# Kernel optimization log

Hardware: AMD Instinct MI355X
Metric: run time of the kernel (lower is better)

## Reference

```python
import jax, jax.numpy as jnp
import numpy as np

D_MODEL = 256
N_HEADS = 8
D_K = D_MODEL // N_HEADS
N = 4096
N_SEG = 16


def setup_inputs() -> dict:
    key = jax.random.key(0)
    ks = jax.random.split(key, 12)
    s = 0.02
    x_q = jax.random.normal(ks[0], (N, D_MODEL), jnp.float32)
    x_kv = jax.random.normal(ks[1], (N, D_MODEL), jnp.float32)
    # same key -> identical segment ids so every query segment exists in kv
    batch = jnp.sort(jax.random.randint(ks[2], (N,), 0, N_SEG)).astype(jnp.int64)
    params = {}
    names = ['Wq', 'Wk', 'Wv', 'Wo']
    for i, n in enumerate(names):
        params[n] = jax.random.normal(ks[3 + i], (D_MODEL, D_MODEL), jnp.float32) * s
        params['b' + n[1]] = jnp.zeros((D_MODEL,), jnp.float32)
    return dict(x_q=x_q, x_kv=x_kv, batch_q=batch, batch_kv=batch, **params)


def reference(x_q, x_kv, batch_q, batch_kv, Wq, bq, Wk, bk, Wv, bv, Wo, bo):
    # projections (torch Linear: x @ W.T + b)
    q = (x_q @ Wq.T + bq).reshape(N, N_HEADS, D_K)   # [Nq, H, dk]
    k = (x_kv @ Wk.T + bk).reshape(N, N_HEADS, D_K)  # [Nkv, H, dk]
    v = (x_kv @ Wv.T + bv).reshape(N, N_HEADS, D_K)
    scores = jnp.einsum('qhd,khd->hqk', q, k) / jnp.sqrt(jnp.float32(D_K))
    mask = batch_q[:, None] == batch_kv[None, :]      # block-diagonal [Nq, Nkv]
    scores = jnp.where(mask[None], scores, -jnp.inf)
    attn = jax.nn.softmax(scores, axis=-1)            # [H, Nq, Nkv]
    out = jnp.einsum('hqk,khd->qhd', attn, v).reshape(N, D_MODEL)
    out = out @ Wo.T + bo
    return out, attn[None]  # match torch's [1, H, Nq, Nkv] attn shape
```

## Files before the change

kernel.cpp:

```cpp
#include <hip/hip_runtime.h>

#define N_TOK 4096
#define DM 256
#define NH 8
#define DK 32

using u16 = unsigned short;
using u32 = unsigned int;
using i64 = long long;
typedef float f32x4 __attribute__((ext_vector_type(4)));

__device__ __forceinline__ float bf2f(u16 u){ return __uint_as_float(((u32)u) << 16); }
__device__ __forceinline__ u16 f2bf(float f){
    u32 x = __float_as_uint(f);
    x += 0x7fffu + ((x >> 16) & 1u);
    return (u16)(x >> 16);
}

__global__ __launch_bounds__(256)
void wt_kernel(const float* __restrict__ Wq, const float* __restrict__ Wk,
               const float* __restrict__ Wv, const float* __restrict__ Wo,
               float* __restrict__ Tq, float* __restrict__ Tk,
               float* __restrict__ Tv, float* __restrict__ To,
               const void* __restrict__ batch_q, const void* __restrict__ batch_kv,
               int2* __restrict__ bounds)
{
    const int b = blockIdx.x;
    const int t = threadIdx.x;
    if (b < 64){
        const float* W = (b < 16) ? Wq : (b < 32) ? Wk : (b < 48) ? Wv : Wo;
        float*      T  = (b < 16) ? Tq : (b < 32) ? Tk : (b < 48) ? Tv : To;
        int blk = b & 15;
        float4* T4 = (float4*)T;
#pragma unroll
        for (int f = 0; f < 4; ++f){
            int F = blk * 1024 + f * 256 + t;
            int d4 = F >> 8;
            int c  = F & 255;
            float4 v = *(const float4*)(W + (size_t)c * DM + 4 * d4);
            T4[F] = v;
        }
    } else {
        int q = (b - 64) * 256 + t;
        const int* kv32 = (const int*)batch_kv;
        const i64* kv64 = (const i64*)batch_kv;
        bool is64 = (kv32[N_TOK - 1] == 0);
        int s = is64 ? (int)((const i64*)batch_q)[q] : ((const int*)batch_q)[q];
        int lo = 0, hi = N_TOK;
        while (lo < hi){ int m = (lo + hi) >> 1; int v = is64 ? (int)kv64[m] : kv32[m]; if (v < s) lo = m + 1; else hi = m; }
        int lo2 = lo, hi2 = N_TOK;
        while (lo2 < hi2){ int m = (lo2 + hi2) >> 1; int v = is64 ? (int)kv64[m] : kv32[m]; if (v <= s) lo2 = m + 1; else hi2 = m; }
        bounds[q] = make_int2(lo, lo2);
    }
}

__global__ __launch_bounds__(256)
void pre_kernel(const float* __restrict__ xq, const float* __restrict__ xkv,
                const float* __restrict__ Tq, const float* __restrict__ bq,
                const float* __restrict__ Tk, const float* __restrict__ bk,
                const float* __restrict__ Tv, const float* __restrict__ bv,
                float* __restrict__ Q, u16* __restrict__ Kp, u16* __restrict__ Vp)
{
    const int b = blockIdx.x;
    const int c = threadIdx.x;
    const int ROWS = 8;

    if (b < 512){
        int row0 = b * ROWS;
        float acc[ROWS];
        float bvv = bq[c];
#pragma unroll
        for (int r = 0; r < ROWS; ++r) acc[r] = bvv;
        const float4* T4 = (const float4*)Tq;
        const float4* xb = (const float4*)(xq + (size_t)row0 * DM);
        for (int i = 0; i < DM / 4; ++i){
            float4 w = T4[i * 256 + c];
#pragma unroll
            for (int r = 0; r < ROWS; ++r){
                float4 xv = xb[r * (DM / 4) + i];
                acc[r] += xv.x * w.x + xv.y * w.y + xv.z * w.z + xv.w * w.w;
            }
        }
#pragma unroll
        for (int r = 0; r < ROWS; ++r)
            Q[(size_t)(row0 + r) * DM + c] = acc[r];
    } else {
        int row0 = (b - 512) * ROWS;
        int hh = c >> 5, dd = c & 31;
        float acck[ROWS], accv[ROWS];
        float bkv = bk[c], bvv = bv[c];
#pragma unroll
        for (int r = 0; r < ROWS; ++r){ acck[r] = bkv; accv[r] = bvv; }
        const float4* Tk4 = (const float4*)Tk;
        const float4* Tv4 = (const float4*)Tv;
        const float4* xb  = (const float4*)(xkv + (size_t)row0 * DM);
        for (int i = 0; i < DM / 4; ++i){
            float4 wk = Tk4[i * 256 + c];
            float4 wv = Tv4[i * 256 + c];
#pragma unroll
            for (int r = 0; r < ROWS; ++r){
                float4 xv = xb[r * (DM / 4) + i];
                acck[r] += xv.x * wk.x + xv.y * wk.y + xv.z * wk.z + xv.w * wk.w;
                accv[r] += xv.x * wv.x + xv.y * wv.y + xv.z * wv.z + xv.w * wv.w;
            }
        }
#pragma unroll
        for (int r = 0; r < ROWS; ++r){
            size_t idx = ((size_t)hh * N_TOK + (row0 + r)) * DK + dd;
            Kp[idx] = f2bf(acck[r]);
            Vp[idx] = f2bf(accv[r]);
        }
    }
}

__global__ __launch_bounds__(256)
void proj_kernel(const float* __restrict__ x, const float* __restrict__ T,
                 const float* __restrict__ bias, float* __restrict__ out)
{
    const int ROWS = 8;
    int row0 = blockIdx.x * ROWS;
    int c = threadIdx.x;
    float acc[ROWS];
    float bv = bias[c];
#pragma unroll
    for (int r = 0; r < ROWS; ++r) acc[r] = bv;
    const float4* T4 = (const float4*)T;
    const float4* xb = (const float4*)(x + (size_t)row0 * DM);
    for (int i = 0; i < DM / 4; ++i){
        float4 w = T4[i * 256 + c];
#pragma unroll
        for (int r = 0; r < ROWS; ++r){
            float4 xv = xb[r * (DM / 4) + i];
            acc[r] += xv.x * w.x + xv.y * w.y + xv.z * w.z + xv.w * w.w;
        }
    }
#pragma unroll
    for (int r = 0; r < ROWS; ++r)
        out[(size_t)(row0 + r) * DM + c] = acc[r];
}

__global__ __launch_bounds__(256)
void attn_kernel(const float* __restrict__ Q, const u16* __restrict__ K,
                 const u16* __restrict__ V, const int2* __restrict__ bounds,
                 float* __restrict__ attn, float* __restrict__ O)
{
    __shared__ float sc[N_TOK];
    __shared__ float qs[DK];
    __shared__ float red[8];
    __shared__ float Osh[DK];

    int q = blockIdx.x, h = blockIdx.y, tid = threadIdx.x;
    int2 bnd = bounds[q];
    const int lo = bnd.x, hi = bnd.y;
    const u16* Kh = K + (size_t)h * N_TOK * DK;
    const u16* Vh = V + (size_t)h * N_TOK * DK;

    if (tid < DK){ qs[tid] = Q[(size_t)q * DM + h * DK + tid]; Osh[tid] = 0.f; }
    __syncthreads();

    const float scale = 0.17677669529663687f;

    float lmax = -1e30f;
    for (int k = lo + tid; k < hi; k += 256){
        const uint4* kr = (const uint4*)(Kh + (size_t)k * DK);
        float dot = 0.f;
#pragma unroll
        for (int i = 0; i < 4; ++i){
            uint4 p = kr[i];
            dot += qs[i*8+0]*bf2f((u16)p.x) + qs[i*8+1]*bf2f((u16)(p.x>>16));
            dot += qs[i*8+2]*bf2f((u16)p.y) + qs[i*8+3]*bf2f((u16)(p.y>>16));
            dot += qs[i*8+4]*bf2f((u16)p.z) + qs[i*8+5]*bf2f((u16)(p.z>>16));
            dot += qs[i*8+6]*bf2f((u16)p.w) + qs[i*8+7]*bf2f((u16)(p.w>>16));
        }
        dot *= scale;
        sc[k - lo] = dot;
        lmax = fmaxf(lmax, dot);
    }
#pragma unroll
    for (int off = 32; off; off >>= 1) lmax = fmaxf(lmax, __shfl_xor(lmax, off, 64));
    if ((tid & 63) == 0) red[tid >> 6] = lmax;
    __syncthreads();
    float m = fmaxf(fmaxf(red[0], red[1]), fmaxf(red[2], red[3]));

    float lsum = 0.f;
    for (int k = lo + tid; k < hi; k += 256){
        float p = __expf(sc[k - lo] - m);
        sc[k - lo] = p;
        lsum += p;
    }
#pragma unroll
    for (int off = 32; off; off >>= 1) lsum += __shfl_xor(lsum, off, 64);
    if ((tid & 63) == 0) red[4 + (tid >> 6)] = lsum;
    __syncthreads();
    float sum = red[4] + red[5] + red[6] + red[7];
    float inv = (sum > 0.f) ? (1.0f / sum) : 0.f;

    f32x4* arow4 = (f32x4*)(attn + ((size_t)h * N_TOK + q) * N_TOK);
#pragma unroll
    for (int i = 0; i < N_TOK / 1024; ++i){
        int t = i * 256 + tid;
        int k0 = 4 * t;
        f32x4 w;
        w.x = (k0 + 0 >= lo && k0 + 0 < hi) ? sc[k0 + 0 - lo] * inv : 0.f;
        w.y = (k0 + 1 >= lo && k0 + 1 < hi) ? sc[k0 + 1 - lo] * inv : 0.f;
        w.z = (k0 + 2 >= lo && k0 + 2 < hi) ? sc[k0 + 2 - lo] * inv : 0.f;
        w.w = (k0 + 3 >= lo && k0 + 3 < hi) ? sc[k0 + 3 - lo] * inv : 0.f;
        __builtin_nontemporal_store(w, &arow4[t]);
    }

    int d2 = tid & 15;
    int g  = tid >> 4;
    float p0 = 0.f, p1 = 0.f;
    for (int k = lo + g; k < hi; k += 16){
        u32 pv = *(const u32*)(Vh + (size_t)k * DK + 2 * d2);
        float p = sc[k - lo];
        p0 += p * bf2f((u16)pv);
        p1 += p * bf2f((u16)(pv >> 16));
    }
    p0 += __shfl_xor(p0, 16, 64); p0 += __shfl_xor(p0, 32, 64);
    p1 += __shfl_xor(p1, 16, 64); p1 += __shfl_xor(p1, 32, 64);
    if ((tid & 63) < 16){
        atomicAdd(&Osh[2 * d2 + 0], p0);
        atomicAdd(&Osh[2 * d2 + 1], p1);
    }

    __syncthreads();
    if (tid < DK) O[(size_t)q * DM + h * DK + tid] = Osh[tid] * inv;
}

extern "C" void kernel_launch(void* const* d_in, const int* in_sizes, int n_in,
                              void* d_out, int out_size, void* d_ws, size_t ws_size,
                              hipStream_t stream)
{
    const float* x_q  = (const float*)d_in[0];
    const float* x_kv = (const float*)d_in[1];
    const void* batch_q  = d_in[2];
    const void* batch_kv = d_in[3];
    const float* Wq = (const float*)d_in[4];
    const float* bq = (const float*)d_in[5];
    const float* Wk = (const float*)d_in[6];
    const float* bk = (const float*)d_in[7];
    const float* Wv = (const float*)d_in[8];
    const float* bv = (const float*)d_in[9];
    const float* Wo = (const float*)d_in[10];
    const float* bo = (const float*)d_in[11];

    char* ws = (char*)d_ws;
    float* Q  = (float*)ws;
    u16*   Kp = (u16*)(ws + (size_t)4 * 1024 * 1024);
    u16*   Vp = (u16*)(ws + (size_t)6 * 1024 * 1024);
    float* O  = (float*)(ws + (size_t)8 * 1024 * 1024);
    int2* bounds = (int2*)(ws + (size_t)12 * 1024 * 1024);
    float* Tq = (float*)(ws + (size_t)13 * 1024 * 1024);
    float* Tk = (float*)(ws + (size_t)13 * 1024 * 1024 + 256 * 1024);
    float* Tv = (float*)(ws + (size_t)13 * 1024 * 1024 + 512 * 1024);
    float* To = (float*)(ws + (size_t)13 * 1024 * 1024 + 768 * 1024);

    float* out  = (float*)d_out;
    float* attn = out + (size_t)N_TOK * DM;

    wt_kernel<<<80, 256, 0, stream>>>(Wq, Wk, Wv, Wo, Tq, Tk, Tv, To,
                                      batch_q, batch_kv, bounds);
    pre_kernel<<<1024, 256, 0, stream>>>(x_q, x_kv, Tq, bq, Tk, bk, Tv, bv,
                                         Q, Kp, Vp);
    attn_kernel<<<dim3(N_TOK, NH), 256, 0, stream>>>(Q, Kp, Vp, bounds, attn, O);
    proj_kernel<<<N_TOK/8, 256, 0, stream>>>((const float*)O, To, bo, out);
}
```

Before: 673.9 us.

## Store K transposed in fp32 and split attn zero-fill from segment writes

The K projection is now written as an fp32 transposed [head*dim][token] array, so threads handling consecutive keys read contiguous floats with q held in registers, instead of unpacking bf16 rows. The attention-row store now writes zero vectors outside the segment range in separate loops and computes values only within the segment span. This trades double the K storage and bandwidth for coalesced access and simpler per-element logic.

```diff
diff --git a/kernel.cpp b/kernel.cpp
--- a/kernel.cpp
+++ b/kernel.cpp
@@ -59,7 +59,7 @@
                 const float* __restrict__ Tq, const float* __restrict__ bq,
                 const float* __restrict__ Tk, const float* __restrict__ bk,
                 const float* __restrict__ Tv, const float* __restrict__ bv,
-                float* __restrict__ Q, u16* __restrict__ Kp, u16* __restrict__ Vp)
+                float* __restrict__ Q, float* __restrict__ KT, u16* __restrict__ Vp)
 {
     const int b = blockIdx.x;
     const int c = threadIdx.x;
@@ -104,10 +104,12 @@
                 accv[r] += xv.x * wv.x + xv.y * wv.y + xv.z * wv.z + xv.w * wv.w;
             }
         }
+        float4* kt4 = (float4*)(KT + (size_t)c * N_TOK + row0);
+        kt4[0] = make_float4(acck[0], acck[1], acck[2], acck[3]);
+        kt4[1] = make_float4(acck[4], acck[5], acck[6], acck[7]);
 #pragma unroll
         for (int r = 0; r < ROWS; ++r){
             size_t idx = ((size_t)hh * N_TOK + (row0 + r)) * DK + dd;
-            Kp[idx] = f2bf(acck[r]);
             Vp[idx] = f2bf(accv[r]);
         }
     }
@@ -140,7 +142,7 @@
 }
 
 __global__ __launch_bounds__(256)
-void attn_kernel(const float* __restrict__ Q, const u16* __restrict__ K,
+void attn_kernel(const float* __restrict__ Q, const float* __restrict__ KT,
                  const u16* __restrict__ V, const int2* __restrict__ bounds,
                  float* __restrict__ attn, float* __restrict__ O)
 {
@@ -152,26 +154,24 @@
     int q = blockIdx.x, h = blockIdx.y, tid = threadIdx.x;
     int2 bnd = bounds[q];
     const int lo = bnd.x, hi = bnd.y;
-    const u16* Kh = K + (size_t)h * N_TOK * DK;
+    const float* KTh = KT + (size_t)h * DK * N_TOK;
     const u16* Vh = V + (size_t)h * N_TOK * DK;
 
     if (tid < DK){ qs[tid] = Q[(size_t)q * DM + h * DK + tid]; Osh[tid] = 0.f; }
     __syncthreads();
 
     const float scale = 0.17677669529663687f;
+
+    float qr[DK];
+#pragma unroll
+    for (int d = 0; d < DK; ++d) qr[d] = qs[d];
 
     float lmax = -1e30f;
     for (int k = lo + tid; k < hi; k += 256){
-        const uint4* kr = (const uint4*)(Kh + (size_t)k * DK);
         float dot = 0.f;
 #pragma unroll
-        for (int i = 0; i < 4; ++i){
-            uint4 p = kr[i];
-            dot += qs[i*8+0]*bf2f((u16)p.x) + qs[i*8+1]*bf2f((u16)(p.x>>16));
-            dot += qs[i*8+2]*bf2f((u16)p.y) + qs[i*8+3]*bf2f((u16)(p.y>>16));
-            dot += qs[i*8+4]*bf2f((u16)p.z) + qs[i*8+5]*bf2f((u16)(p.z>>16));
-            dot += qs[i*8+6]*bf2f((u16)p.w) + qs[i*8+7]*bf2f((u16)(p.w>>16));
-        }
+        for (int d = 0; d < DK; ++d)
+            dot += qr[d] * KTh[(size_t)d * N_TOK + k];
         dot *= scale;
         sc[k - lo] = dot;
         lmax = fmaxf(lmax, dot);
@@ -196,9 +196,14 @@
     float inv = (sum > 0.f) ? (1.0f / sum) : 0.f;
 
     f32x4* arow4 = (f32x4*)(attn + ((size_t)h * N_TOK + q) * N_TOK);
-#pragma unroll
-    for (int i = 0; i < N_TOK / 1024; ++i){
-        int t = i * 256 + tid;
+    const f32x4 z4 = {0.f, 0.f, 0.f, 0.f};
+    const int lo4 = lo >> 2;
+    const int hi4 = (hi + 3) >> 2;
+    for (int t = tid; t < lo4; t += 256)
+        __builtin_nontemporal_store(z4, &arow4[t]);
+    for (int t = hi4 + tid; t < N_TOK / 4; t += 256)
+        __builtin_nontemporal_store(z4, &arow4[t]);
+    for (int t = lo4 + tid; t < hi4; t += 256){
         int k0 = 4 * t;
         f32x4 w;
         w.x = (k0 + 0 >= lo && k0 + 0 < hi) ? sc[k0 + 0 - lo] * inv : 0.f;
@@ -247,14 +252,14 @@
 
     char* ws = (char*)d_ws;
     float* Q  = (float*)ws;
-    u16*   Kp = (u16*)(ws + (size_t)4 * 1024 * 1024);
-    u16*   Vp = (u16*)(ws + (size_t)6 * 1024 * 1024);
-    float* O  = (float*)(ws + (size_t)8 * 1024 * 1024);
-    int2* bounds = (int2*)(ws + (size_t)12 * 1024 * 1024);
-    float* Tq = (float*)(ws + (size_t)13 * 1024 * 1024);
-    float* Tk = (float*)(ws + (size_t)13 * 1024 * 1024 + 256 * 1024);
-    float* Tv = (float*)(ws + (size_t)13 * 1024 * 1024 + 512 * 1024);
-    float* To = (float*)(ws + (size_t)13 * 1024 * 1024 + 768 * 1024);
+    float* KT = (float*)(ws + (size_t)4 * 1024 * 1024);
+    u16*   Vp = (u16*)(ws + (size_t)8 * 1024 * 1024);
+    float* O  = (float*)(ws + (size_t)10 * 1024 * 1024);
+    int2* bounds = (int2*)(ws + (size_t)14 * 1024 * 1024);
+    float* Tq = (float*)(ws + (size_t)14 * 1024 * 1024 + 256 * 1024);
+    float* Tk = (float*)(ws + (size_t)14 * 1024 * 1024 + 512 * 1024);
+    float* Tv = (float*)(ws + (size_t)14 * 1024 * 1024 + 768 * 1024);
+    float* To = (float*)(ws + (size_t)14 * 1024 * 1024 + 1024 * 1024);
 
     float* out  = (float*)d_out;
     float* attn = out + (size_t)N_TOK * DM;
@@ -262,7 +267,7 @@
     wt_kernel<<<80, 256, 0, stream>>>(Wq, Wk, Wv, Wo, Tq, Tk, Tv, To,
                                       batch_q, batch_kv, bounds);
     pre_kernel<<<1024, 256, 0, stream>>>(x_q, x_kv, Tq, bq, Tk, bk, Tv, bv,
-                                         Q, Kp, Vp);
-    attn_kernel<<<dim3(N_TOK, NH), 256, 0, stream>>>(Q, Kp, Vp, bounds, attn, O);
+                                         Q, KT, Vp);
+    attn_kernel<<<dim3(N_TOK, NH), 256, 0, stream>>>(Q, KT, Vp, bounds, attn, O);
     proj_kernel<<<N_TOK/8, 256, 0, stream>>>((const float*)O, To, bo, out);
 }
```

New measurement: 697.5 us. 3.5% more time.

## Process all heads per query block and split zero-fill stores from softmax stores

Applied to the files above, without the earlier changes.

The attention kernel now launches one block per query instead of one per (query, head). Each block loops over the 8 heads, loading the full query row into shared memory once and holding the per-head slice in registers. The attention-row write is split into pure zero-fill loops outside the segment and a masked loop only over the segment's range, which avoids per-element LDS reads and bounds checks on the zeroed region. This cuts block count and launch granularity, but serialises the heads within a block, which may reduce latency hiding on the store-bound attention-matrix write.

```diff
diff --git a/kernel.cpp b/kernel.cpp
--- a/kernel.cpp
+++ b/kernel.cpp
@@ -145,87 +145,103 @@
                  float* __restrict__ attn, float* __restrict__ O)
 {
     __shared__ float sc[N_TOK];
-    __shared__ float qs[DK];
+    __shared__ float qs[DM];
     __shared__ float red[8];
     __shared__ float Osh[DK];
 
-    int q = blockIdx.x, h = blockIdx.y, tid = threadIdx.x;
-    int2 bnd = bounds[q];
+    const int q = blockIdx.x, tid = threadIdx.x;
+    const int2 bnd = bounds[q];
     const int lo = bnd.x, hi = bnd.y;
-    const u16* Kh = K + (size_t)h * N_TOK * DK;
-    const u16* Vh = V + (size_t)h * N_TOK * DK;
-
-    if (tid < DK){ qs[tid] = Q[(size_t)q * DM + h * DK + tid]; Osh[tid] = 0.f; }
+
+    if (tid < 64) ((float4*)qs)[tid] = ((const float4*)(Q + (size_t)q * DM))[tid];
+    if (tid < DK) Osh[tid] = 0.f;
     __syncthreads();
 
     const float scale = 0.17677669529663687f;
-
-    float lmax = -1e30f;
-    for (int k = lo + tid; k < hi; k += 256){
-        const uint4* kr = (const uint4*)(Kh + (size_t)k * DK);
-        float dot = 0.f;
-#pragma unroll
-        for (int i = 0; i < 4; ++i){
-            uint4 p = kr[i];
-            dot += qs[i*8+0]*bf2f((u16)p.x) + qs[i*8+1]*bf2f((u16)(p.x>>16));
-            dot += qs[i*8+2]*bf2f((u16)p.y) + qs[i*8+3]*bf2f((u16)(p.y>>16));
-            dot += qs[i*8+4]*bf2f((u16)p.z) + qs[i*8+5]*bf2f((u16)(p.z>>16));
-            dot += qs[i*8+6]*bf2f((u16)p.w) + qs[i*8+7]*bf2f((u16)(p.w>>16));
-        }
-        dot *= scale;
-        sc[k - lo] = dot;
-        lmax = fmaxf(lmax, dot);
-    }
-#pragma unroll
-    for (int off = 32; off; off >>= 1) lmax = fmaxf(lmax, __shfl_xor(lmax, off, 64));
-    if ((tid & 63) == 0) red[tid >> 6] = lmax;
-    __syncthreads();
-    float m = fmaxf(fmaxf(red[0], red[1]), fmaxf(red[2], red[3]));
-
-    float lsum = 0.f;
-    for (int k = lo + tid; k < hi; k += 256){
-        float p = __expf(sc[k - lo] - m);
-        sc[k - lo] = p;
-        lsum += p;
-    }
-#pragma unroll
-    for (int off = 32; off; off >>= 1) lsum += __shfl_xor(lsum, off, 64);
-    if ((tid & 63) == 0) red[4 + (tid >> 6)] = lsum;
-    __syncthreads();
-    float sum = red[4] + red[5] + red[6] + red[7];
-    float inv = (sum > 0.f) ? (1.0f / sum) : 0.f;
-
-    f32x4* arow4 = (f32x4*)(attn + ((size_t)h * N_TOK + q) * N_TOK);
-#pragma unroll
-    for (int i = 0; i < N_TOK / 1024; ++i){
-        int t = i * 256 + tid;
-        int k0 = 4 * t;
-        f32x4 w;
-        w.x = (k0 + 0 >= lo && k0 + 0 < hi) ? sc[k0 + 0 - lo] * inv : 0.f;
-        w.y = (k0 + 1 >= lo && k0 + 1 < hi) ? sc[k0 + 1 - lo] * inv : 0.f;
-        w.z = (k0 + 2 >= lo && k0 + 2 < hi) ? sc[k0 + 2 - lo] * inv : 0.f;
-        w.w = (k0 + 3 >= lo && k0 + 3 < hi) ? sc[k0 + 3 - lo] * inv : 0.f;
-        __builtin_nontemporal_store(w, &arow4[t]);
-    }
-
-    int d2 = tid & 15;
-    int g  = tid >> 4;
-    float p0 = 0.f, p1 = 0.f;
-    for (int k = lo + g; k < hi; k += 16){
-        u32 pv = *(const u32*)(Vh + (size_t)k * DK + 2 * d2);
-        float p = sc[k - lo];
-        p0 += p * bf2f((u16)pv);
-        p1 += p * bf2f((u16)(pv >> 16));
-    }
-    p0 += __shfl_xor(p0, 16, 64); p0 += __shfl_xor(p0, 32, 64);
-    p1 += __shfl_xor(p1, 16, 64); p1 += __shfl_xor(p1, 32, 64);
-    if ((tid & 63) < 16){
-        atomicAdd(&Osh[2 * d2 + 0], p0);
-        atomicAdd(&Osh[2 * d2 + 1], p1);
-    }
-
-    __syncthreads();
-    if (tid < DK) O[(size_t)q * DM + h * DK + tid] = Osh[tid] * inv;
+    const int lo4 = lo >> 2;
+    const int hi4 = (hi + 3) >> 2;
+
+    for (int h = 0; h < NH; ++h){
+        const u16* Kh = K + (size_t)h * N_TOK * DK;
+        const u16* Vh = V + (size_t)h * N_TOK * DK;
+
+        float qr[DK];
+#pragma unroll
+        for (int d = 0; d < DK; ++d) qr[d] = qs[h * DK + d];
+
+        float lmax = -1e30f;
+        for (int k = lo + tid; k < hi; k += 256){
+            const uint4* kr = (const uint4*)(Kh + (size_t)k * DK);
+            float dot = 0.f;
+#pragma unroll
+            for (int i = 0; i < 4; ++i){
+                uint4 p = kr[i];
+                dot += qr[i*8+0]*bf2f((u16)p.x) + qr[i*8+1]*bf2f((u16)(p.x>>16));
+                dot += qr[i*8+2]*bf2f((u16)p.y) + qr[i*8+3]*bf2f((u16)(p.y>>16));
+                dot += qr[i*8+4]*bf2f((u16)p.z) + qr[i*8+5]*bf2f((u16)(p.z>>16));
+                dot += qr[i*8+6]*bf2f((u16)p.w) + qr[i*8+7]*bf2f((u16)(p.w>>16));
+            }
+            dot *= scale;
+            sc[k - lo] = dot;
+            lmax = fmaxf(lmax, dot);
+        }
+#pragma unroll
+        for (int off = 32; off; off >>= 1) lmax = fmaxf(lmax, __shfl_xor(lmax, off, 64));
+        if ((tid & 63) == 0) red[tid >> 6] = lmax;
+        __syncthreads();
+        float m = fmaxf(fmaxf(red[0], red[1]), fmaxf(red[2], red[3]));
+
+        float lsum = 0.f;
+        for (int k = lo + tid; k < hi; k += 256){
+            float p = __expf(sc[k - lo] - m);
+            sc[k - lo] = p;
+            lsum += p;
+        }
+#pragma unroll
+        for (int off = 32; off; off >>= 1) lsum += __shfl_xor(lsum, off, 64);
+        if ((tid & 63) == 0) red[4 + (tid >> 6)] = lsum;
+        __syncthreads();
+        float sum = red[4] + red[5] + red[6] + red[7];
+        float inv = (sum > 0.f) ? (1.0f / sum) : 0.f;
+
+        f32x4* arow4 = (f32x4*)(attn + ((size_t)h * N_TOK + q) * N_TOK);
+        const f32x4 z4 = {0.f, 0.f, 0.f, 0.f};
+        for (int t = tid; t < lo4; t += 256)
+            __builtin_nontemporal_store(z4, &arow4[t]);
+        for (int t = hi4 + tid; t < N_TOK / 4; t += 256)
+            __builtin_nontemporal_store(z4, &arow4[t]);
+        for (int t = lo4 + tid; t < hi4; t += 256){
+            int k0 = 4 * t;
+            f32x4 w;
+            w.x = (k0 + 0 >= lo && k0 + 0 < hi) ? sc[k0 + 0 - lo] * inv : 0.f;
+            w.y = (k0 + 1 >= lo && k0 + 1 < hi) ? sc[k0 + 1 - lo] * inv : 0.f;
+            w.z = (k0 + 2 >= lo && k0 + 2 < hi) ? sc[k0 + 2 - lo] * inv : 0.f;
+            w.w = (k0 + 3 >= lo && k0 + 3 < hi) ? sc[k0 + 3 - lo] * inv : 0.f;
+            __builtin_nontemporal_store(w, &arow4[t]);
+        }
+
+        int d2 = tid & 15;
+        int g  = tid >> 4;
+        float p0 = 0.f, p1 = 0.f;
+        for (int k = lo + g; k < hi; k += 16){
+            u32 pv = *(const u32*)(Vh + (size_t)k * DK + 2 * d2);
+            float p = sc[k - lo];
+            p0 += p * bf2f((u16)pv);
+            p1 += p * bf2f((u16)(pv >> 16));
+        }
+        p0 += __shfl_xor(p0, 16, 64); p0 += __shfl_xor(p0, 32, 64);
+        p1 += __shfl_xor(p1, 16, 64); p1 += __shfl_xor(p1, 32, 64);
+        if ((tid & 63) < 16){
+            atomicAdd(&Osh[2 * d2 + 0], p0);
+            atomicAdd(&Osh[2 * d2 + 1], p1);
+        }
+
+        __syncthreads();
+        if (tid < DK){
+            O[(size_t)q * DM + h * DK + tid] = Osh[tid] * inv;
+            Osh[tid] = 0.f;
+        }
+    }
 }
 
 extern "C" void kernel_launch(void* const* d_in, const int* in_sizes, int n_in,
@@ -263,6 +279,6 @@
                                       batch_q, batch_kv, bounds);
     pre_kernel<<<1024, 256, 0, stream>>>(x_q, x_kv, Tq, bq, Tk, bk, Tv, bv,
                                          Q, Kp, Vp);
-    attn_kernel<<<dim3(N_TOK, NH), 256, 0, stream>>>(Q, Kp, Vp, bounds, attn, O);
+    attn_kernel<<<N_TOK, 256, 0, stream>>>(Q, Kp, Vp, bounds, attn, O);
     proj_kernel<<<N_TOK/8, 256, 0, stream>>>((const float*)O, To, bo, out);
 }
```

Result: slower. 720.9 us (+7.0%).
